# Kernel optimization log

Measured on AMD Instinct MI355X. Metric: run time of the kernel, lower is better.

Reference implementation:

```python
import jax, jax.numpy as jnp
import numpy as np

B, N, D = 2, 2048, 1024
H, QH, DH = 8, 16, 64        # kv heads, query heads, head dim
SOFTCLAMP = 50.0


def setup_inputs() -> dict:
    key = jax.random.key(0)
    ks = jax.random.split(key, 7)
    return {
        "tokens": jax.random.normal(ks[0], (B, N, D), jnp.float32),
        "norm_w": jnp.ones((D,), jnp.float32) + 0.02 * jax.random.normal(ks[1], (D,), jnp.float32),
        "Wq":  0.02 * jax.random.normal(ks[2], (D, QH * DH), jnp.float32),
        "Wkv": 0.02 * jax.random.normal(ks[3], (D, 2 * H * DH), jnp.float32),
        "Wout": 0.02 * jax.random.normal(ks[4], (H * DH, D), jnp.float32),
        "q_gamma": 0.02 * jax.random.normal(ks[5], (QH, DH), jnp.float32),
        "k_gamma": 0.02 * jax.random.normal(ks[6], (H, DH), jnp.float32),
    }


def _rmsnorm(x, w):
    eps = jnp.finfo(x.dtype).eps
    return x * jax.lax.rsqrt(jnp.mean(x * x, axis=-1, keepdims=True) + eps) * w


def _l2norm(x):
    # F.normalize(dim=-1, p=2) clamps the norm at eps=1e-12
    n = jnp.maximum(jnp.linalg.norm(x, axis=-1, keepdims=True), 1e-12)
    return x / n


def _mh_rmsnorm(x, gamma):
    # x: [b, h, n, d]; gamma: [h, d]; scale = (gamma + 1) * sqrt(d)
    scale = (gamma + 1.0) * np.sqrt(x.shape[-1]).astype(np.float32)
    return _l2norm(x) * scale[None, :, None, :]


def reference(tokens, norm_w, Wq, Wkv, Wout, q_gamma, k_gamma):
    b, n, d = tokens.shape
    x = _rmsnorm(tokens, norm_w)

    q = (x @ Wq).reshape(b, n, QH, DH).transpose(0, 2, 1, 3)      # [b, QH, n, dh]
    kv = x @ Wkv
    k = kv[..., : H * DH].reshape(b, n, H, DH).transpose(0, 2, 1, 3)  # [b, H, n, dh]
    v = kv[..., H * DH:].reshape(b, n, H, DH).transpose(0, 2, 1, 3)   # [b, H, n, dh]

    q = _mh_rmsnorm(q, q_gamma)
    k = _mh_rmsnorm(k, k_gamma)

    g = QH // H
    q = q.reshape(b, H, g, n, DH)                                 # [b, h, g, i, dh]

    sim = jnp.einsum('bhgid,bhjd->bhgij', q, k)                   # [b, h, g, i, j]
    sim = jnp.tanh(sim / SOFTCLAMP) * SOFTCLAMP                   # softcap BEFORE scale (faithful)
    sim = sim * (DH ** -0.5)

    neg = -jnp.finfo(sim.dtype).max
    causal = jnp.triu(jnp.ones((n, n), dtype=bool), 1)
    sim = jnp.where(causal, neg, sim)

    attn = jax.nn.softmax(sim, axis=-1)
    # NOTE: original einsum sums over the group axis g -> [b, h, i, dh]
    out = jnp.einsum('bhgij,bhjd->bhid', attn, v)
    out = out.transpose(0, 2, 1, 3).reshape(b, n, H * DH)
    return out @ Wout
```

## Files before the change

### kernel.cpp

```cpp
#include <hip/hip_runtime.h>
#include <hip/hip_bf16.h>
#include <type_traits>

typedef unsigned short u16;
typedef __attribute__((ext_vector_type(2))) float f32x2;
typedef __attribute__((ext_vector_type(4))) float f32x4;
typedef __attribute__((ext_vector_type(8))) short short8;
typedef __attribute__((ext_vector_type(4))) short short4v;
typedef __attribute__((ext_vector_type(8))) __bf16 bf16x8;
typedef __attribute__((ext_vector_type(4))) __bf16 bf16x4;

#define BB 2
#define NN 2048
#define DDIM 1024
#define HH 8
#define QHH 16
#define DHH 64

__device__ __forceinline__ float b2f(u16 v) {
    return __builtin_bit_cast(float, ((unsigned)v) << 16);
}
__device__ __forceinline__ u16 f2b(float f) {
    unsigned u = __builtin_bit_cast(unsigned, f);
    u += 0x7FFFu + ((u >> 16) & 1u);
    return (u16)(u >> 16);
}
__device__ __forceinline__ float fastrcp(float x) {
#if __has_builtin(__builtin_amdgcn_rcpf)
    return __builtin_amdgcn_rcpf(x);
#else
    return 1.0f / x;
#endif
}
__device__ __forceinline__ float fastexp2(float x) {
#if __has_builtin(__builtin_amdgcn_exp2f)
    return __builtin_amdgcn_exp2f(x);
#else
    return exp2f(x);
#endif
}
__device__ __forceinline__ f32x2 sp2(float v) { return (f32x2){v, v}; }
__device__ __forceinline__ f32x4 mfma16(short8 a, short8 b, f32x4 c) {
    return __builtin_amdgcn_mfma_f32_16x16x32_bf16(
        __builtin_bit_cast(bf16x8, a), __builtin_bit_cast(bf16x8, b), c, 0, 0, 0);
}
#if __has_builtin(__builtin_amdgcn_mfma_f32_16x16x16_bf16)
__device__ __forceinline__ f32x4 mfma_k16(short4v a, short4v b, f32x4 c) {
    return __builtin_amdgcn_mfma_f32_16x16x16_bf16(
        __builtin_bit_cast(bf16x4, a), __builtin_bit_cast(bf16x4, b), c, 0, 0, 0);
}
#else
__device__ __forceinline__ f32x4 mfma_k16(short4v a, short4v b, f32x4 c) {
    return __builtin_amdgcn_mfma_f32_16x16x16bf16_1k(a, b, c, 0, 0, 0);
}
#endif
__device__ __forceinline__ void stage16(const u16* g, u16* l, int lane) {
#if __has_builtin(__builtin_amdgcn_global_load_lds)
    __builtin_amdgcn_global_load_lds(
        (const __attribute__((address_space(1))) unsigned int*)g,
        (__attribute__((address_space(3))) unsigned int*)l, 16, 0, 0);
#else
    *(short8*)(l + lane * 8) = *(const short8*)g;
#endif
}

__global__ __launch_bounds__(256) void k_rmsnorm(const float* __restrict__ tokens,
                                                 const float* __restrict__ norm_w,
                                                 u16* __restrict__ xb) {
    const int row = blockIdx.x;
    const int tid = threadIdx.x;
    const float* xp = tokens + (size_t)row * DDIM + tid * 4;
    float4 raw = *(const float4*)xp;
    float ss = raw.x * raw.x + raw.y * raw.y + raw.z * raw.z + raw.w * raw.w;
#pragma unroll
    for (int d = 1; d < 64; d <<= 1) ss += __shfl_xor(ss, d);
    __shared__ float red[4];
    if ((tid & 63) == 0) red[tid >> 6] = ss;
    __syncthreads();
    float tot = red[0] + red[1] + red[2] + red[3];
    float r = rsqrtf(tot * (1.0f / 1024.0f) + 1.1920929e-7f);
    float4 wv = *(const float4*)(norm_w + tid * 4);
    ushort4 o;
    o.x = f2b(raw.x * r * wv.x);
    o.y = f2b(raw.y * r * wv.y);
    o.z = f2b(raw.z * r * wv.z);
    o.w = f2b(raw.w * r * wv.w);
    *(ushort4*)(xb + (size_t)row * DDIM + tid * 4) = o;
}

__global__ __launch_bounds__(256) void k_wprep(const float* __restrict__ Wq,
                                               const float* __restrict__ Wkv,
                                               const float* __restrict__ Wout,
                                               u16* __restrict__ WqT,
                                               u16* __restrict__ WkvT,
                                               u16* __restrict__ WoutT) {
    const int z = blockIdx.z;
    const float* in = (z == 0) ? Wq : (z == 1) ? Wkv : Wout;
    u16* out = (z == 0) ? WqT : (z == 1) ? WkvT : WoutT;
    const int R = (z == 2) ? 512 : 1024, C = 1024;
    const int br = blockIdx.y * 32;
    if (br >= R) return;
    __shared__ u16 tile[32][33];
    const int bc = blockIdx.x * 32;
    const int tx = threadIdx.x & 31, ty = threadIdx.x >> 5;
#pragma unroll
    for (int i = 0; i < 32; i += 8) tile[ty + i][tx] = f2b(in[(size_t)(br + ty + i) * C + bc + tx]);
    __syncthreads();
#pragma unroll
    for (int i = 0; i < 32; i += 8) out[(size_t)(bc + ty + i) * R + br + tx] = tile[tx][ty + i];
}

__global__ __launch_bounds__(256) void k_gemm128(const u16* __restrict__ A,
                                                 const u16* __restrict__ Bt,
                                                 u16* __restrict__ C,
                                                 int M, int Ncols, int K) {
    __shared__ __attribute__((aligned(16))) u16 As[128 * 32];
    __shared__ __attribute__((aligned(16))) u16 Bs[128 * 32];
    const int tid = threadIdx.x;
    const int lane = tid & 63;
    const int w = tid >> 6;
    const int m0 = blockIdx.y * 128;
    const int n0 = blockIdx.x * 128;
    const int wr = (w >> 1) * 64;
    const int wc = (w & 1) * 64;
    const int lr = lane & 15;
    const int lq = lane >> 4;

    const int ch0 = w * 32;
    const u16* aSrc = A + (size_t)(m0 + ch0 + (lane >> 2)) * K + (lane & 3) * 8;
    const u16* bSrc = Bt + (size_t)(n0 + ch0 + (lane >> 2)) * K + (lane & 3) * 8;
    u16* aDst = As + ch0 * 32;
    u16* bDst = Bs + ch0 * 32;

    f32x4 acc[4][4];
#pragma unroll
    for (int i = 0; i < 4; i++)
#pragma unroll
        for (int j = 0; j < 4; j++) acc[i][j] = (f32x4){0.f, 0.f, 0.f, 0.f};

    for (int k0 = 0; k0 < K; k0 += 32) {
        __syncthreads();
        stage16(aSrc, aDst, lane);
        stage16(aSrc + (size_t)16 * K, aDst + 512, lane);
        stage16(bSrc, bDst, lane);
        stage16(bSrc + (size_t)16 * K, bDst + 512, lane);
        aSrc += 32;
        bSrc += 32;
        __syncthreads();
        short8 a[4], b[4];
#pragma unroll
        for (int mi = 0; mi < 4; ++mi) a[mi] = *(const short8*)&As[(wr + mi * 16 + lr) * 32 + lq * 8];
#pragma unroll
        for (int ni = 0; ni < 4; ++ni) b[ni] = *(const short8*)&Bs[(wc + ni * 16 + lr) * 32 + lq * 8];
#pragma unroll
        for (int mi = 0; mi < 4; ++mi)
#pragma unroll
            for (int ni = 0; ni < 4; ++ni) acc[mi][ni] = mfma16(a[mi], b[ni], acc[mi][ni]);
    }
#pragma unroll
    for (int mi = 0; mi < 4; ++mi)
#pragma unroll
        for (int ni = 0; ni < 4; ++ni)
#pragma unroll
            for (int r = 0; r < 4; ++r) {
                int row = m0 + wr + mi * 16 + lq * 4 + r;
                int col = n0 + wc + ni * 16 + lr;
                C[(size_t)row * Ncols + col] = f2b(acc[mi][ni][r]);
            }
}

__global__ __launch_bounds__(256) void k_gemm64f(const u16* __restrict__ A,
                                                 const u16* __restrict__ Bt,
                                                 float* __restrict__ C,
                                                 int M, int Ncols, int K) {
    __shared__ __attribute__((aligned(16))) u16 As[64 * 32];
    __shared__ __attribute__((aligned(16))) u16 Bs[128 * 32];
    const int tid = threadIdx.x;
    const int lane = tid & 63;
    const int w = tid >> 6;
    const int m0 = blockIdx.y * 64;
    const int n0 = blockIdx.x * 128;
    const int lr = lane & 15;
    const int lq = lane >> 4;

    const u16* aSrc = A + (size_t)(m0 + w * 16 + (lane >> 2)) * K + (lane & 3) * 8;
    const u16* bSrc = Bt + (size_t)(n0 + w * 32 + (lane >> 2)) * K + (lane & 3) * 8;
    u16* aDst = As + w * 16 * 32;
    u16* bDst = Bs + w * 32 * 32;

    f32x4 acc[8];
#pragma unroll
    for (int i = 0; i < 8; i++) acc[i] = (f32x4){0.f, 0.f, 0.f, 0.f};

    for (int k0 = 0; k0 < K; k0 += 32) {
        __syncthreads();
        stage16(aSrc, aDst, lane);
        stage16(bSrc, bDst, lane);
        stage16(bSrc + (size_t)16 * K, bDst + 512, lane);
        aSrc += 32;
        bSrc += 32;
        __syncthreads();
        short8 a = *(const short8*)&As[(w * 16 + lr) * 32 + lq * 8];
#pragma unroll
        for (int nt = 0; nt < 8; ++nt) {
            short8 b = *(const short8*)&Bs[(nt * 16 + lr) * 32 + lq * 8];
            acc[nt] = mfma16(a, b, acc[nt]);
        }
    }
#pragma unroll
    for (int nt = 0; nt < 8; ++nt)
#pragma unroll
        for (int r = 0; r < 4; ++r) {
            int row = m0 + w * 16 + lq * 4 + r;
            int col = n0 + nt * 16 + lr;
            C[(size_t)row * Ncols + col] = acc[nt][r];
        }
}

__global__ __launch_bounds__(256) void k_headnorm(const u16* __restrict__ qkv,
                                                  const float* __restrict__ q_gamma,
                                                  const float* __restrict__ k_gamma,
                                                  u16* __restrict__ qn,
                                                  u16* __restrict__ kn) {
    const int row = blockIdx.x;
    const int b = row >> 11, n = row & 2047;
    const int lane = threadIdx.x & 63, w = threadIdx.x >> 6;
    const u16* qr = qkv + (size_t)row * 2048;
    const u16* kvr = qkv + (size_t)row * 2048 + 1024;
#pragma unroll
    for (int t = 0; t < 4; ++t) {
        int qh = w * 4 + t;
        float v = b2f(qr[qh * 64 + lane]);
        float ss = v * v;
#pragma unroll
        for (int d = 1; d < 64; d <<= 1) ss += __shfl_xor(ss, d);
        float nrm = fmaxf(sqrtf(ss), 1e-12f);
        float g = q_gamma[qh * 64 + lane];
        qn[((size_t)(b * QHH + qh) * NN + n) * 64 + lane] = f2b(v / nrm * (g + 1.0f) * 8.0f);
    }
#pragma unroll
    for (int t = 0; t < 2; ++t) {
        int kh = w * 2 + t;
        float v = b2f(kvr[kh * 64 + lane]);
        float ss = v * v;
#pragma unroll
        for (int d = 1; d < 64; d <<= 1) ss += __shfl_xor(ss, d);
        float nrm = fmaxf(sqrtf(ss), 1e-12f);
        float g = k_gamma[kh * 64 + lane];
        kn[((size_t)(b * HH + kh) * NN + n) * 64 + lane] = f2b(v / nrm * (g + 1.0f) * 0.16f);
    }
}

__global__ __launch_bounds__(256) void k_vtrans(const u16* __restrict__ qkv,
                                                u16* __restrict__ vt) {
    const int bh = blockIdx.x;
    const int b = bh >> 3, h = bh & 7;
    const int n0 = blockIdx.y * 64;
    const int tid = threadIdx.x;
    __shared__ u16 t[64 * 72];
#pragma unroll
    for (int it = 0; it < 2; ++it) {
        int idx = tid + it * 256;
        int i = idx >> 3, c = idx & 7;
        short8 v = *(const short8*)&qkv[(size_t)(b * NN + n0 + i) * 2048 + 1536 + h * 64 + c * 8];
        *(short8*)&t[i * 72 + c * 8] = v;
    }
    __syncthreads();
#pragma unroll
    for (int it = 0; it < 2; ++it) {
        int idx = tid + it * 256;
        int d = idx >> 3, c = idx & 7;
        u16 tmp[8];
#pragma unroll
        for (int j = 0; j < 8; ++j) tmp[j] = t[(c * 8 + j) * 72 + d];
        *(short8*)&vt[((size_t)(bh * 64 + d)) * NN + n0 + c * 8] = *(short8*)tmp;
    }
}

__global__ __launch_bounds__(256) void k_attn(const u16* __restrict__ qn,
                                              const u16* __restrict__ kn,
                                              const u16* __restrict__ vt,
                                              u16* __restrict__ OT) {
    const int bq = blockIdx.x;
    const int b = bq >> 4, qh = bq & 15;
    const int h = qh >> 1;
    const int tid = threadIdx.x;
    const int lane = tid & 63, w = tid >> 6;
    const int lr = lane & 15, lq = lane >> 4;
    const int z = 31 - blockIdx.y;
    const int i0 = z * 64 + w * 16;
    const int ntile = z + 1;

    const u16* Qp = qn + (size_t)(b * QHH + qh) * NN * 64;
    const u16* Kp = kn + (size_t)(b * HH + h) * NN * 64;
    const u16* Vp = vt + (size_t)(b * HH + h) * 64 * NN;
    u16* Op = OT + (size_t)(b * QHH + qh) * 64 * NN;

    __shared__ __attribute__((aligned(16))) u16 Ks[2][64 * 64];
    __shared__ __attribute__((aligned(16))) u16 Vs[2][64 * 64];

    short8 qf0 = *(const short8*)&Qp[(size_t)(i0 + lr) * 64 + lq * 8];
    short8 qf1 = *(const short8*)&Qp[(size_t)(i0 + lr) * 64 + 32 + lq * 8];

    f32x4 of[4];
#pragma unroll
    for (int dt = 0; dt < 4; ++dt) of[dt] = (f32x4){0.f, 0.f, 0.f, 0.f};
    f32x4 lacc = (f32x4){0.f, 0.f, 0.f, 0.f};
    const int irow = i0 + lr;

    const short4v ones4 = {(short)0x3F80, (short)0x3F80, (short)0x3F80, (short)0x3F80};

    const int srow = lane >> 3;
    const int sch = (lane ^ srow) & 7;
    const int rA = w * 16, rB = w * 16 + 8;

    const u16* kSrcA = Kp + (size_t)(rA + srow) * 64 + sch * 8;
    const u16* kSrcB = Kp + (size_t)(rB + srow) * 64 + sch * 8;
    const u16* vSrcA = Vp + (size_t)(rA + srow) * NN + sch * 8;
    const u16* vSrcB = Vp + (size_t)(rB + srow) * NN + sch * 8;

    auto stageKV = [&](int buf) {
        stage16(kSrcA, &Ks[buf][rA * 64], lane);
        stage16(kSrcB, &Ks[buf][rB * 64], lane);
        stage16(vSrcA, &Vs[buf][rA * 64], lane);
        stage16(vSrcB, &Vs[buf][rB * 64], lane);
        kSrcA += 64 * 64;
        kSrcB += 64 * 64;
        vSrcA += 64;
        vSrcB += 64;
    };

    auto tile = [&](int buf, int jt) {
        const int j0 = jt << 6;
        const u16* kb = &Ks[buf][0];
        const u16* vb = &Vs[buf][0];
        f32x4 sc[4];
#pragma unroll
        for (int ct = 0; ct < 4; ++ct) {
            const int r = ct * 16 + lr;
            short8 kf0 = *(const short8*)&kb[r * 64 + ((lq ^ (lr & 7)) << 3)];
            short8 kf1 = *(const short8*)&kb[r * 64 + (((4 + lq) ^ (lr & 7)) << 3)];
            f32x4 t = (f32x4){0.f, 0.f, 0.f, 0.f};
            t = mfma16(kf0, qf0, t);
            t = mfma16(kf1, qf1, t);
            sc[ct] = t;
        }
        const bool masked = (jt == ntile - 1);
        short4v pk[4];
#pragma unroll
        for (int ct = 0; ct < 4; ++ct) {
            const int lim = irow - (j0 + ct * 16 + lq * 4);
            f32x2 xa = {sc[ct][0], sc[ct][1]};
            f32x2 xb = {sc[ct][2], sc[ct][3]};
            f32x2 ya = xa * xa;
            f32x2 yb = xb * xb;
            f32x2 Ga = __builtin_elementwise_fma(ya, __builtin_elementwise_fma(ya,
                           __builtin_elementwise_fma(ya, __builtin_elementwise_fma(ya,
                               sp2(0.04705711f), sp2(-0.32327190f)), sp2(1.11500760f)),
                           sp2(-2.98719110f)), sp2(9.01599730f));
            f32x2 Gb = __builtin_elementwise_fma(yb, __builtin_elementwise_fma(yb,
                           __builtin_elementwise_fma(yb, __builtin_elementwise_fma(yb,
                               sp2(0.04705711f), sp2(-0.32327190f)), sp2(1.11500760f)),
                           sp2(-2.98719110f)), sp2(9.01599730f));
            f32x2 aa = __builtin_elementwise_fma(xa, Ga, sp2(-9.0168440f));
            f32x2 ab = __builtin_elementwise_fma(xb, Gb, sp2(-9.0168440f));
            float p0 = fastexp2(aa.x);
            float p1 = fastexp2(aa.y);
            float p2 = fastexp2(ab.x);
            float p3 = fastexp2(ab.y);
            if (masked) {
                p0 = (0 <= lim) ? p0 : 0.0f;
                p1 = (1 <= lim) ? p1 : 0.0f;
                p2 = (2 <= lim) ? p2 : 0.0f;
                p3 = (3 <= lim) ? p3 : 0.0f;
            }
            bf16x4 pb;
            pb[0] = (__bf16)p0;
            pb[1] = (__bf16)p1;
            pb[2] = (__bf16)p2;
            pb[3] = (__bf16)p3;
            pk[ct] = __builtin_bit_cast(short4v, pb);
        }
#pragma unroll
        for (int ct = 0; ct < 4; ++ct) lacc = mfma_k16(ones4, pk[ct], lacc);
#pragma unroll
        for (int dt = 0; dt < 4; ++dt) {
            const int d = dt * 16 + lr;
#pragma unroll
            for (int ct = 0; ct < 4; ++ct) {
                short4v vf = *(const short4v*)
                    &vb[d * 64 + ((((ct << 1) + (lq >> 1)) ^ (lr & 7)) << 3) + ((lq & 1) << 2)];
                of[dt] = mfma_k16(vf, pk[ct], of[dt]);
            }
        }
    };

    stageKV(0);
    for (int jt = 0; jt < ntile; ++jt) {
        const int buf = jt & 1;
        __syncthreads();
        if (jt + 1 < ntile) stageKV(buf ^ 1);
        tile(buf, jt);
    }

    const float inv = fastrcp(lacc[0]);
#pragma unroll
    for (int dt = 0; dt < 4; ++dt)
#pragma unroll
        for (int r = 0; r < 4; ++r)
            Op[(size_t)(dt * 16 + lq * 4 + r) * NN + irow] = f2b(of[dt][r] * inv);
}

__global__ __launch_bounds__(256) void k_gsum(const u16* __restrict__ OT, u16* __restrict__ AO) {
    __shared__ u16 t[32][34];
    const int b = blockIdx.z;
    const int n0 = blockIdx.x * 32;
    const int c0 = blockIdx.y * 32;
    const int hh = c0 >> 6, d0 = c0 & 63;
    const int tx = threadIdx.x & 31, ty = threadIdx.x >> 5;
    const u16* O0 = OT + ((size_t)(b * QHH + 2 * hh) * 64 + d0) * NN;
    const u16* O1 = OT + ((size_t)(b * QHH + 2 * hh + 1) * 64 + d0) * NN;
#pragma unroll
    for (int i = ty; i < 32; i += 8)
        t[i][tx] = f2b(b2f(O0[(size_t)i * NN + n0 + tx]) + b2f(O1[(size_t)i * NN + n0 + tx]));
    __syncthreads();
#pragma unroll
    for (int i = ty; i < 32; i += 8)
        AO[((size_t)(b * NN) + n0 + i) * 512 + c0 + tx] = t[tx][i];
}

extern "C" void kernel_launch(void* const* d_in, const int* in_sizes, int n_in,
                              void* d_out, int out_size, void* d_ws, size_t ws_size,
                              hipStream_t stream) {
    const float* tokens = (const float*)d_in[0];
    const float* norm_w = (const float*)d_in[1];
    const float* Wq = (const float*)d_in[2];
    const float* Wkv = (const float*)d_in[3];
    const float* Wout = (const float*)d_in[4];
    const float* q_gamma = (const float*)d_in[5];
    const float* k_gamma = (const float*)d_in[6];
    float* out = (float*)d_out;

    char* ws = (char*)d_ws;
    u16* xb = (u16*)(ws + 0);
    u16* WqT = (u16*)(ws + 8388608);
    u16* WkvT = (u16*)(ws + 10485760);
    u16* WoutT = (u16*)(ws + 12582912);
    u16* qkv = (u16*)(ws + 13631488);
    u16* kn = (u16*)(ws + 30408704);
    u16* vtb = (u16*)(ws + 34603008);
    u16* qn = xb;
    u16* Obuf = qkv;
    u16* AO = (u16*)(ws + 22020096);

    k_rmsnorm<<<4096, 256, 0, stream>>>(tokens, norm_w, xb);
    k_wprep<<<dim3(32, 32, 3), 256, 0, stream>>>(Wq, Wkv, Wout, WqT, WkvT, WoutT);
    k_gemm128<<<dim3(16, 32), 256, 0, stream>>>(xb, WqT, qkv, 4096, 2048, 1024);
    k_headnorm<<<4096, 256, 0, stream>>>(qkv, q_gamma, k_gamma, qn, kn);
    k_vtrans<<<dim3(16, 32), 256, 0, stream>>>(qkv, vtb);
    k_attn<<<dim3(32, 32), 256, 0, stream>>>(qn, kn, vtb, Obuf);
    k_gsum<<<dim3(64, 16, 2), 256, 0, stream>>>(Obuf, AO);
    k_gemm64f<<<dim3(8, 64), 256, 0, stream>>>(AO, WoutT, out, 4096, 1024, 512);
}
```

Before: 187.8 us.

## Process both GQA query heads per attention block to share K/V tiles

Each attention block now handles both query heads of a KV group. Every K/V tile staged into shared memory feeds two sets of score and PV MFMAs, which halves the K/V global and LDS traffic and the grid size. The softmax row sum moves from a ones-vector MFMA to a VALU accumulation with cross-lane shuffles. The mapping from blockIdx.y to causal row tile is also reordered. In exchange, per-thread register pressure roughly doubles, which may cut occupancy. Block-level load balance also changes, because there are fewer, heavier blocks and small tiles are now dispatched first.

```diff
diff --git a/kernel.cpp b/kernel.cpp
--- a/kernel.cpp
+++ b/kernel.cpp
@@ -281,34 +281,39 @@
                                               const u16* __restrict__ kn,
                                               const u16* __restrict__ vt,
                                               u16* __restrict__ OT) {
-    const int bq = blockIdx.x;
-    const int b = bq >> 4, qh = bq & 15;
-    const int h = qh >> 1;
+    const int bh = blockIdx.x;
+    const int b = bh >> 3, h = bh & 7;
     const int tid = threadIdx.x;
     const int lane = tid & 63, w = tid >> 6;
     const int lr = lane & 15, lq = lane >> 4;
-    const int z = 31 - blockIdx.y;
+    const int y = blockIdx.y;
+    const int z = (y < 16) ? y : 47 - y;
     const int i0 = z * 64 + w * 16;
     const int ntile = z + 1;
-
-    const u16* Qp = qn + (size_t)(b * QHH + qh) * NN * 64;
+    const int irow = i0 + lr;
+
+    const u16* Qp0 = qn + (size_t)(b * QHH + 2 * h) * NN * 64;
+    const u16* Qp1 = Qp0 + (size_t)NN * 64;
     const u16* Kp = kn + (size_t)(b * HH + h) * NN * 64;
     const u16* Vp = vt + (size_t)(b * HH + h) * 64 * NN;
-    u16* Op = OT + (size_t)(b * QHH + qh) * 64 * NN;
+    u16* Op0 = OT + (size_t)(b * QHH + 2 * h) * 64 * NN;
+    u16* Op1 = Op0 + (size_t)64 * NN;
 
     __shared__ __attribute__((aligned(16))) u16 Ks[2][64 * 64];
     __shared__ __attribute__((aligned(16))) u16 Vs[2][64 * 64];
 
-    short8 qf0 = *(const short8*)&Qp[(size_t)(i0 + lr) * 64 + lq * 8];
-    short8 qf1 = *(const short8*)&Qp[(size_t)(i0 + lr) * 64 + 32 + lq * 8];
-
-    f32x4 of[4];
-#pragma unroll
-    for (int dt = 0; dt < 4; ++dt) of[dt] = (f32x4){0.f, 0.f, 0.f, 0.f};
-    f32x4 lacc = (f32x4){0.f, 0.f, 0.f, 0.f};
-    const int irow = i0 + lr;
-
-    const short4v ones4 = {(short)0x3F80, (short)0x3F80, (short)0x3F80, (short)0x3F80};
+    short8 qA0 = *(const short8*)&Qp0[(size_t)(i0 + lr) * 64 + lq * 8];
+    short8 qA1 = *(const short8*)&Qp0[(size_t)(i0 + lr) * 64 + 32 + lq * 8];
+    short8 qB0 = *(const short8*)&Qp1[(size_t)(i0 + lr) * 64 + lq * 8];
+    short8 qB1 = *(const short8*)&Qp1[(size_t)(i0 + lr) * 64 + 32 + lq * 8];
+
+    f32x4 ofA[4], ofB[4];
+#pragma unroll
+    for (int dt = 0; dt < 4; ++dt) {
+        ofA[dt] = (f32x4){0.f, 0.f, 0.f, 0.f};
+        ofB[dt] = (f32x4){0.f, 0.f, 0.f, 0.f};
+    }
+    f32x2 lsA = {0.f, 0.f}, lsB = {0.f, 0.f};
 
     const int srow = lane >> 3;
     const int sch = (lane ^ srow) & 7;
@@ -330,59 +335,68 @@
         vSrcB += 64;
     };
 
+    auto smax = [&](f32x4 sc, int lim, bool masked, f32x2& ls) -> short4v {
+        f32x2 xa = {sc[0], sc[1]};
+        f32x2 xb = {sc[2], sc[3]};
+        f32x2 ya = xa * xa;
+        f32x2 yb = xb * xb;
+        f32x2 Ga = __builtin_elementwise_fma(ya, __builtin_elementwise_fma(ya,
+                       __builtin_elementwise_fma(ya, __builtin_elementwise_fma(ya,
+                           sp2(0.04705711f), sp2(-0.32327190f)), sp2(1.11500760f)),
+                       sp2(-2.98719110f)), sp2(9.01599730f));
+        f32x2 Gb = __builtin_elementwise_fma(yb, __builtin_elementwise_fma(yb,
+                       __builtin_elementwise_fma(yb, __builtin_elementwise_fma(yb,
+                           sp2(0.04705711f), sp2(-0.32327190f)), sp2(1.11500760f)),
+                       sp2(-2.98719110f)), sp2(9.01599730f));
+        f32x2 aa = __builtin_elementwise_fma(xa, Ga, sp2(-9.0168440f));
+        f32x2 ab = __builtin_elementwise_fma(xb, Gb, sp2(-9.0168440f));
+        float p0 = fastexp2(aa.x);
+        float p1 = fastexp2(aa.y);
+        float p2 = fastexp2(ab.x);
+        float p3 = fastexp2(ab.y);
+        if (masked) {
+            p0 = (0 <= lim) ? p0 : 0.0f;
+            p1 = (1 <= lim) ? p1 : 0.0f;
+            p2 = (2 <= lim) ? p2 : 0.0f;
+            p3 = (3 <= lim) ? p3 : 0.0f;
+        }
+        ls += (f32x2){p0, p1};
+        ls += (f32x2){p2, p3};
+        bf16x4 pb;
+        pb[0] = (__bf16)p0;
+        pb[1] = (__bf16)p1;
+        pb[2] = (__bf16)p2;
+        pb[3] = (__bf16)p3;
+        return __builtin_bit_cast(short4v, pb);
+    };
+
     auto tile = [&](int buf, int jt) {
         const int j0 = jt << 6;
         const u16* kb = &Ks[buf][0];
         const u16* vb = &Vs[buf][0];
-        f32x4 sc[4];
+        f32x4 scA[4], scB[4];
 #pragma unroll
         for (int ct = 0; ct < 4; ++ct) {
             const int r = ct * 16 + lr;
             short8 kf0 = *(const short8*)&kb[r * 64 + ((lq ^ (lr & 7)) << 3)];
             short8 kf1 = *(const short8*)&kb[r * 64 + (((4 + lq) ^ (lr & 7)) << 3)];
-            f32x4 t = (f32x4){0.f, 0.f, 0.f, 0.f};
-            t = mfma16(kf0, qf0, t);
-            t = mfma16(kf1, qf1, t);
-            sc[ct] = t;
+            f32x4 tA = (f32x4){0.f, 0.f, 0.f, 0.f};
+            tA = mfma16(kf0, qA0, tA);
+            tA = mfma16(kf1, qA1, tA);
+            scA[ct] = tA;
+            f32x4 tB = (f32x4){0.f, 0.f, 0.f, 0.f};
+            tB = mfma16(kf0, qB0, tB);
+            tB = mfma16(kf1, qB1, tB);
+            scB[ct] = tB;
         }
         const bool masked = (jt == ntile - 1);
-        short4v pk[4];
+        short4v pkA[4], pkB[4];
 #pragma unroll
         for (int ct = 0; ct < 4; ++ct) {
             const int lim = irow - (j0 + ct * 16 + lq * 4);
-            f32x2 xa = {sc[ct][0], sc[ct][1]};
-            f32x2 xb = {sc[ct][2], sc[ct][3]};
-            f32x2 ya = xa * xa;
-            f32x2 yb = xb * xb;
-            f32x2 Ga = __builtin_elementwise_fma(ya, __builtin_elementwise_fma(ya,
-                           __builtin_elementwise_fma(ya, __builtin_elementwise_fma(ya,
-                               sp2(0.04705711f), sp2(-0.32327190f)), sp2(1.11500760f)),
-                           sp2(-2.98719110f)), sp2(9.01599730f));
-            f32x2 Gb = __builtin_elementwise_fma(yb, __builtin_elementwise_fma(yb,
-                           __builtin_elementwise_fma(yb, __builtin_elementwise_fma(yb,
-                               sp2(0.04705711f), sp2(-0.32327190f)), sp2(1.11500760f)),
-                           sp2(-2.98719110f)), sp2(9.01599730f));
-            f32x2 aa = __builtin_elementwise_fma(xa, Ga, sp2(-9.0168440f));
-            f32x2 ab = __builtin_elementwise_fma(xb, Gb, sp2(-9.0168440f));
-            float p0 = fastexp2(aa.x);
-            float p1 = fastexp2(aa.y);
-            float p2 = fastexp2(ab.x);
-            float p3 = fastexp2(ab.y);
-            if (masked) {
-                p0 = (0 <= lim) ? p0 : 0.0f;
-                p1 = (1 <= lim) ? p1 : 0.0f;
-                p2 = (2 <= lim) ? p2 : 0.0f;
-                p3 = (3 <= lim) ? p3 : 0.0f;
-            }
-            bf16x4 pb;
-            pb[0] = (__bf16)p0;
-            pb[1] = (__bf16)p1;
-            pb[2] = (__bf16)p2;
-            pb[3] = (__bf16)p3;
-            pk[ct] = __builtin_bit_cast(short4v, pb);
-        }
-#pragma unroll
-        for (int ct = 0; ct < 4; ++ct) lacc = mfma_k16(ones4, pk[ct], lacc);
+            pkA[ct] = smax(scA[ct], lim, masked, lsA);
+            pkB[ct] = smax(scB[ct], lim, masked, lsB);
+        }
 #pragma unroll
         for (int dt = 0; dt < 4; ++dt) {
             const int d = dt * 16 + lr;
@@ -390,7 +404,8 @@
             for (int ct = 0; ct < 4; ++ct) {
                 short4v vf = *(const short4v*)
                     &vb[d * 64 + ((((ct << 1) + (lq >> 1)) ^ (lr & 7)) << 3) + ((lq & 1) << 2)];
-                of[dt] = mfma_k16(vf, pk[ct], of[dt]);
+                ofA[dt] = mfma_k16(vf, pkA[ct], ofA[dt]);
+                ofB[dt] = mfma_k16(vf, pkB[ct], ofB[dt]);
             }
         }
     };
@@ -403,12 +418,21 @@
         tile(buf, jt);
     }
 
-    const float inv = fastrcp(lacc[0]);
+    float lA = lsA.x + lsA.y;
+    lA += __shfl_xor(lA, 16);
+    lA += __shfl_xor(lA, 32);
+    float lB = lsB.x + lsB.y;
+    lB += __shfl_xor(lB, 16);
+    lB += __shfl_xor(lB, 32);
+    const float invA = fastrcp(lA);
+    const float invB = fastrcp(lB);
 #pragma unroll
     for (int dt = 0; dt < 4; ++dt)
 #pragma unroll
-        for (int r = 0; r < 4; ++r)
-            Op[(size_t)(dt * 16 + lq * 4 + r) * NN + irow] = f2b(of[dt][r] * inv);
+        for (int r = 0; r < 4; ++r) {
+            Op0[(size_t)(dt * 16 + lq * 4 + r) * NN + irow] = f2b(ofA[dt][r] * invA);
+            Op1[(size_t)(dt * 16 + lq * 4 + r) * NN + irow] = f2b(ofB[dt][r] * invB);
+        }
 }
 
 __global__ __launch_bounds__(256) void k_gsum(const u16* __restrict__ OT, u16* __restrict__ AO) {
@@ -458,7 +482,7 @@
     k_gemm128<<<dim3(16, 32), 256, 0, stream>>>(xb, WqT, qkv, 4096, 2048, 1024);
     k_headnorm<<<4096, 256, 0, stream>>>(qkv, q_gamma, k_gamma, qn, kn);
     k_vtrans<<<dim3(16, 32), 256, 0, stream>>>(qkv, vtb);
-    k_attn<<<dim3(32, 32), 256, 0, stream>>>(qn, kn, vtb, Obuf);
+    k_attn<<<dim3(16, 32), 256, 0, stream>>>(qn, kn, vtb, Obuf);
     k_gsum<<<dim3(64, 16, 2), 256, 0, stream>>>(Obuf, AO);
     k_gemm64f<<<dim3(8, 64), 256, 0, stream>>>(AO, WoutT, out, 4096, 1024, 512);
 }
```

After: 204.7 us. +9.0%, slower.

## Share K/V tiles across the query-head pair in 512-thread attention blocks

Applied to the files above, without the earlier changes.

The attention kernel now launches one 512-thread block per (batch, kv head, query tile), so the two query heads of a GQA group use the same K/V tiles staged in shared memory. Each wave stages half as much K/V as before. The launch order of query tiles is changed so long and short causal tiles interleave. The row-sum MFMA against a ones vector is replaced by per-lane float accumulation followed by cross-lane shuffles. The cost is bigger blocks with fewer of them, which may lower occupancy and scheduling flexibility.

```diff
diff --git a/kernel.cpp b/kernel.cpp
--- a/kernel.cpp
+++ b/kernel.cpp
@@ -277,24 +277,27 @@
     }
 }
 
-__global__ __launch_bounds__(256) void k_attn(const u16* __restrict__ qn,
+__global__ __launch_bounds__(512) void k_attn(const u16* __restrict__ qn,
                                               const u16* __restrict__ kn,
                                               const u16* __restrict__ vt,
                                               u16* __restrict__ OT) {
-    const int bq = blockIdx.x;
-    const int b = bq >> 4, qh = bq & 15;
-    const int h = qh >> 1;
+    const int bh = blockIdx.x;
+    const int b = bh >> 3, h = bh & 7;
     const int tid = threadIdx.x;
     const int lane = tid & 63, w = tid >> 6;
+    const int hsel = w >> 2;
+    const int rg = w & 3;
     const int lr = lane & 15, lq = lane >> 4;
-    const int z = 31 - blockIdx.y;
-    const int i0 = z * 64 + w * 16;
+    const int y = blockIdx.y;
+    const int z = (y < 16) ? (31 - y) : (y - 16);
+    const int i0 = z * 64 + rg * 16;
     const int ntile = z + 1;
-
-    const u16* Qp = qn + (size_t)(b * QHH + qh) * NN * 64;
+    const int irow = i0 + lr;
+
+    const u16* Qp = qn + (size_t)(b * QHH + 2 * h + hsel) * NN * 64;
     const u16* Kp = kn + (size_t)(b * HH + h) * NN * 64;
     const u16* Vp = vt + (size_t)(b * HH + h) * 64 * NN;
-    u16* Op = OT + (size_t)(b * QHH + qh) * 64 * NN;
+    u16* Op = OT + (size_t)(b * QHH + 2 * h + hsel) * 64 * NN;
 
     __shared__ __attribute__((aligned(16))) u16 Ks[2][64 * 64];
     __shared__ __attribute__((aligned(16))) u16 Vs[2][64 * 64];
@@ -305,29 +308,54 @@
     f32x4 of[4];
 #pragma unroll
     for (int dt = 0; dt < 4; ++dt) of[dt] = (f32x4){0.f, 0.f, 0.f, 0.f};
-    f32x4 lacc = (f32x4){0.f, 0.f, 0.f, 0.f};
-    const int irow = i0 + lr;
-
-    const short4v ones4 = {(short)0x3F80, (short)0x3F80, (short)0x3F80, (short)0x3F80};
+    f32x2 ls = {0.f, 0.f};
 
     const int srow = lane >> 3;
     const int sch = (lane ^ srow) & 7;
-    const int rA = w * 16, rB = w * 16 + 8;
-
-    const u16* kSrcA = Kp + (size_t)(rA + srow) * 64 + sch * 8;
-    const u16* kSrcB = Kp + (size_t)(rB + srow) * 64 + sch * 8;
-    const u16* vSrcA = Vp + (size_t)(rA + srow) * NN + sch * 8;
-    const u16* vSrcB = Vp + (size_t)(rB + srow) * NN + sch * 8;
+
+    const u16* kSrc = Kp + (size_t)(w * 8 + srow) * 64 + sch * 8;
+    const u16* vSrc = Vp + (size_t)(w * 8 + srow) * NN + sch * 8;
 
     auto stageKV = [&](int buf) {
-        stage16(kSrcA, &Ks[buf][rA * 64], lane);
-        stage16(kSrcB, &Ks[buf][rB * 64], lane);
-        stage16(vSrcA, &Vs[buf][rA * 64], lane);
-        stage16(vSrcB, &Vs[buf][rB * 64], lane);
-        kSrcA += 64 * 64;
-        kSrcB += 64 * 64;
-        vSrcA += 64;
-        vSrcB += 64;
+        stage16(kSrc, &Ks[buf][w * 8 * 64], lane);
+        stage16(vSrc, &Vs[buf][w * 8 * 64], lane);
+        kSrc += 64 * 64;
+        vSrc += 64;
+    };
+
+    auto smax = [&](f32x4 sc, int lim, bool masked) -> short4v {
+        f32x2 xa = {sc[0], sc[1]};
+        f32x2 xb = {sc[2], sc[3]};
+        f32x2 ya = xa * xa;
+        f32x2 yb = xb * xb;
+        f32x2 Ga = __builtin_elementwise_fma(ya, __builtin_elementwise_fma(ya,
+                       __builtin_elementwise_fma(ya, __builtin_elementwise_fma(ya,
+                           sp2(0.04705711f), sp2(-0.32327190f)), sp2(1.11500760f)),
+                       sp2(-2.98719110f)), sp2(9.01599730f));
+        f32x2 Gb = __builtin_elementwise_fma(yb, __builtin_elementwise_fma(yb,
+                       __builtin_elementwise_fma(yb, __builtin_elementwise_fma(yb,
+                           sp2(0.04705711f), sp2(-0.32327190f)), sp2(1.11500760f)),
+                       sp2(-2.98719110f)), sp2(9.01599730f));
+        f32x2 aa = __builtin_elementwise_fma(xa, Ga, sp2(-9.0168440f));
+        f32x2 ab = __builtin_elementwise_fma(xb, Gb, sp2(-9.0168440f));
+        float p0 = fastexp2(aa.x);
+        float p1 = fastexp2(aa.y);
+        float p2 = fastexp2(ab.x);
+        float p3 = fastexp2(ab.y);
+        if (masked) {
+            p0 = (0 <= lim) ? p0 : 0.0f;
+            p1 = (1 <= lim) ? p1 : 0.0f;
+            p2 = (2 <= lim) ? p2 : 0.0f;
+            p3 = (3 <= lim) ? p3 : 0.0f;
+        }
+        ls += (f32x2){p0, p1};
+        ls += (f32x2){p2, p3};
+        bf16x4 pb;
+        pb[0] = (__bf16)p0;
+        pb[1] = (__bf16)p1;
+        pb[2] = (__bf16)p2;
+        pb[3] = (__bf16)p3;
+        return __builtin_bit_cast(short4v, pb);
     };
 
     auto tile = [&](int buf, int jt) {
@@ -350,39 +378,8 @@
 #pragma unroll
         for (int ct = 0; ct < 4; ++ct) {
             const int lim = irow - (j0 + ct * 16 + lq * 4);
-            f32x2 xa = {sc[ct][0], sc[ct][1]};
-            f32x2 xb = {sc[ct][2], sc[ct][3]};
-            f32x2 ya = xa * xa;
-            f32x2 yb = xb * xb;
-            f32x2 Ga = __builtin_elementwise_fma(ya, __builtin_elementwise_fma(ya,
-                           __builtin_elementwise_fma(ya, __builtin_elementwise_fma(ya,
-                               sp2(0.04705711f), sp2(-0.32327190f)), sp2(1.11500760f)),
-                           sp2(-2.98719110f)), sp2(9.01599730f));
-            f32x2 Gb = __builtin_elementwise_fma(yb, __builtin_elementwise_fma(yb,
-                           __builtin_elementwise_fma(yb, __builtin_elementwise_fma(yb,
-                               sp2(0.04705711f), sp2(-0.32327190f)), sp2(1.11500760f)),
-                           sp2(-2.98719110f)), sp2(9.01599730f));
-            f32x2 aa = __builtin_elementwise_fma(xa, Ga, sp2(-9.0168440f));
-            f32x2 ab = __builtin_elementwise_fma(xb, Gb, sp2(-9.0168440f));
-            float p0 = fastexp2(aa.x);
-            float p1 = fastexp2(aa.y);
-            float p2 = fastexp2(ab.x);
-            float p3 = fastexp2(ab.y);
-            if (masked) {
-                p0 = (0 <= lim) ? p0 : 0.0f;
-                p1 = (1 <= lim) ? p1 : 0.0f;
-                p2 = (2 <= lim) ? p2 : 0.0f;
-                p3 = (3 <= lim) ? p3 : 0.0f;
-            }
-            bf16x4 pb;
-            pb[0] = (__bf16)p0;
-            pb[1] = (__bf16)p1;
-            pb[2] = (__bf16)p2;
-            pb[3] = (__bf16)p3;
-            pk[ct] = __builtin_bit_cast(short4v, pb);
-        }
-#pragma unroll
-        for (int ct = 0; ct < 4; ++ct) lacc = mfma_k16(ones4, pk[ct], lacc);
+            pk[ct] = smax(sc[ct], lim, masked);
+        }
 #pragma unroll
         for (int dt = 0; dt < 4; ++dt) {
             const int d = dt * 16 + lr;
@@ -403,7 +400,10 @@
         tile(buf, jt);
     }
 
-    const float inv = fastrcp(lacc[0]);
+    float l = ls.x + ls.y;
+    l += __shfl_xor(l, 16);
+    l += __shfl_xor(l, 32);
+    const float inv = fastrcp(l);
 #pragma unroll
     for (int dt = 0; dt < 4; ++dt)
 #pragma unroll
@@ -458,7 +458,7 @@
     k_gemm128<<<dim3(16, 32), 256, 0, stream>>>(xb, WqT, qkv, 4096, 2048, 1024);
     k_headnorm<<<4096, 256, 0, stream>>>(qkv, q_gamma, k_gamma, qn, kn);
     k_vtrans<<<dim3(16, 32), 256, 0, stream>>>(qkv, vtb);
-    k_attn<<<dim3(32, 32), 256, 0, stream>>>(qn, kn, vtb, Obuf);
+    k_attn<<<dim3(16, 32), 512, 0, stream>>>(qn, kn, vtb, Obuf);
     k_gsum<<<dim3(64, 16, 2), 256, 0, stream>>>(Obuf, AO);
     k_gemm64f<<<dim3(8, 64), 256, 0, stream>>>(AO, WoutT, out, 4096, 1024, 512);
 }
```

Result: slower. 195.4 us (+4.0%).
